# Optimization experiments

Measured on AMD Instinct MI355X. Metric: run time of the kernel, lower is better.

Reference implementation:

```python
import jax, jax.numpy as jnp
import numpy as np

B, V = 256, 2048
PD, MD, H = 1024, 512, 512

def setup_inputs() -> dict:
    key = jax.random.key(0)
    k1, k2, k3, k4, k5 = jax.random.split(key, 5)
    patient_emb = jax.random.normal(k1, (B, PD), dtype=jnp.float32)
    atc4_emb = jax.random.normal(k2, (V, MD), dtype=jnp.float32)
    # Linear(PD+MD -> H): weight (H, PD+MD), bias (H,)
    W1 = jax.random.normal(k3, (H, PD + MD), dtype=jnp.float32) * 0.02
    b1 = jnp.zeros((H,), dtype=jnp.float32)
    # Linear(H -> 1): weight (1, H) -> store as (H,), bias scalar
    w2 = jax.random.normal(k4, (H,), dtype=jnp.float32) * 0.05
    b2 = jnp.zeros((), dtype=jnp.float32)
    return {"patient_emb": patient_emb, "atc4_emb": atc4_emb,
            "W1": W1, "b1": b1, "w2": w2, "b2": b2}

def reference(patient_emb, atc4_emb, W1, b1, w2, b2):
    # Algebraically equivalent to cat([patient, mol]) @ W1.T:
    # split W1 into patient and mol blocks, matmul each, broadcast-add.
    W1p = W1[:, :PD]   # (H, PD)
    W1m = W1[:, PD:]   # (H, MD)
    hp = jnp.einsum('bp,hp->bh', patient_emb, W1p)   # (B, H)
    hm = jnp.einsum('vm,hm->vh', atc4_emb, W1m)      # (V, H)
    h = jnp.tanh(hp[:, None, :] + hm[None, :, :] + b1)  # (B, V, H)
    scores = jnp.einsum('bvh,h->bv', h, w2) + b2     # (B, V)
    return scores
```

## Files before the change

### kernel.cpp

```cpp
#include <hip/hip_runtime.h>
#include <hip/hip_bf16.h>
#include <math.h>

typedef __attribute__((ext_vector_type(8))) short short8;
typedef __attribute__((ext_vector_type(4))) float float4v;
typedef __attribute__((ext_vector_type(2))) float float2v;

__device__ __forceinline__ float2v lo2(float4v v) {
    return __builtin_shufflevector(v, v, 0, 1);
}
__device__ __forceinline__ float2v hi2(float4v v) {
    return __builtin_shufflevector(v, v, 2, 3);
}

__device__ __forceinline__ int2 cvt2bf16x4(float4v v) {
    union { __hip_bfloat162 h2; int i; } u0, u1;
    u0.h2 = __float22bfloat162_rn(make_float2(v.x, v.y));
    u1.h2 = __float22bfloat162_rn(make_float2(v.z, v.w));
    return make_int2(u0.i, u1.i);
}

__global__ __launch_bounds__(256) void gemm_exp(
    const float* __restrict__ patient, const float* __restrict__ atc4,
    const float* __restrict__ W1, const float* __restrict__ b1,
    float* __restrict__ EA, float* __restrict__ EM)
{
    const float* A; const float* W; const float* bias; float* T;
    int lda, K, M;
    if (blockIdx.z == 0) {
        if (blockIdx.x >= 4) return;
        A = patient; lda = 1024; K = 1024; M = 256; bias = b1; T = EA; W = W1;
    } else {
        A = atc4;    lda = 512;  K = 512;  M = 2048; bias = nullptr; T = EM; W = W1 + 1024;
    }
    const int ldw = 1536;

    __shared__ short As[64][72];
    __shared__ short Bs[64][72];
    const int t = threadIdx.x;
    const int m0 = blockIdx.x * 64;
    const int n0 = blockIdx.y * 64;
    const int wave = t >> 6;
    const int lane = t & 63;
    const int wm = (wave & 1) * 32;
    const int wn = (wave >> 1) * 32;
    const int lrow = lane & 15;
    const int quad = lane >> 4;

    float4v acc[2][2];
    #pragma unroll
    for (int i = 0; i < 2; i++)
        #pragma unroll
        for (int j = 0; j < 2; j++)
            acc[i][j] = (float4v){0.f, 0.f, 0.f, 0.f};

    const int sr = t >> 2;
    const int sc = (t & 3) * 16;

    for (int k0 = 0; k0 < K; k0 += 64) {
        const float* ap = A + (size_t)(m0 + sr) * lda + (k0 + sc);
        const float* wp = W + (size_t)(n0 + sr) * ldw + (k0 + sc);
        #pragma unroll
        for (int ii = 0; ii < 4; ii++) {
            float4v av = *(const float4v*)(ap + ii * 4);
            float4v wv = *(const float4v*)(wp + ii * 4);
            *(int2*)&As[sr][sc + ii * 4] = cvt2bf16x4(av);
            *(int2*)&Bs[sr][sc + ii * 4] = cvt2bf16x4(wv);
        }
        __syncthreads();
        #pragma unroll
        for (int kk = 0; kk < 64; kk += 32) {
            short8 af[2], bfr[2];
            #pragma unroll
            for (int i = 0; i < 2; i++)
                af[i] = *(const short8*)&As[wm + i * 16 + lrow][kk + quad * 8];
            #pragma unroll
            for (int j = 0; j < 2; j++)
                bfr[j] = *(const short8*)&Bs[wn + j * 16 + lrow][kk + quad * 8];
            #pragma unroll
            for (int i = 0; i < 2; i++)
                #pragma unroll
                for (int j = 0; j < 2; j++)
                    acc[i][j] = __builtin_amdgcn_mfma_f32_16x16x32_bf16(
                        af[i], bfr[j], acc[i][j], 0, 0, 0);
        }
        __syncthreads();
    }

    #pragma unroll
    for (int i = 0; i < 2; i++) {
        #pragma unroll
        for (int j = 0; j < 2; j++) {
            const int n  = n0 + wn + j * 16 + lrow;
            const int mb = m0 + wm + i * 16 + quad * 4;
            const float bn = bias ? bias[n] : 0.0f;
            float4v ev;
            #pragma unroll
            for (int r = 0; r < 4; r++)
                ev[r] = __expf(2.0f * (acc[i][j][r] + bn));
            *(float4v*)&T[(size_t)n * M + mb] = ev;
        }
    }
}

__device__ __forceinline__ void rat4(
    float2v em0, float2v em1, float2v em2, float2v em3,
    float2v a0, float2v a1, float2v a2, float2v a3,
    float2v c0, float2v c1, float2v c2, float2v c3,
    float2v& acc)
{
    const float2v one2 = {1.f, 1.f};
    float2v d0 = __builtin_elementwise_fma(em0, a0, one2);
    float2v d1 = __builtin_elementwise_fma(em1, a1, one2);
    float2v d2 = __builtin_elementwise_fma(em2, a2, one2);
    float2v d3 = __builtin_elementwise_fma(em3, a3, one2);
    float2v e01 = d0 * d1;
    float2v e23 = d2 * d3;
    float2v n01 = __builtin_elementwise_fma(d1, c0, d0 * c1);
    float2v n23 = __builtin_elementwise_fma(d3, c2, d2 * c3);
    float2v num = __builtin_elementwise_fma(n01, e23, n23 * e01);
    float2v den = e01 * e23;
    float2v r = { __builtin_amdgcn_rcpf(den.x), __builtin_amdgcn_rcpf(den.y) };
    acc = __builtin_elementwise_fma(num, r, acc);
}

__global__ __launch_bounds__(256) void pair_kernel(
    const float* __restrict__ EA, const float* __restrict__ EM,
    const float* __restrict__ w2, float* __restrict__ partial)
{
    __shared__ float sEA[32][68];
    __shared__ float sEM[32][132];
    __shared__ float4v sC4[16];
    const int t  = threadIdx.x;
    const int v0 = blockIdx.x * 128;
    const int b0 = blockIdx.y * 64;
    const int h0 = blockIdx.z * 64;
    const int tx = t & 15;
    const int ty = t >> 4;

    if (t < 16) {
        float4v wv = *(const float4v*)(w2 + h0 + 4 * t);
        sC4[t] = -2.0f * wv;
    }

    float2v accAL[4], accAH[4], accBL[4], accBH[4];
    #pragma unroll
    for (int i = 0; i < 4; i++) {
        accAL[i] = (float2v){0.f, 0.f};  accAH[i] = (float2v){0.f, 0.f};
        accBL[i] = (float2v){0.f, 0.f};  accBH[i] = (float2v){0.f, 0.f};
    }

    const int rS = t >> 3;
    const int cA = (t & 7) * 8;
    const int cM = (t & 7) * 16;

    float4v pA0, pA1, pM0, pM1, pM2, pM3;
    {
        const float* pa = EA + (size_t)(h0 + rS) * 256 + b0 + cA;
        pA0 = *(const float4v*)pa;  pA1 = *(const float4v*)(pa + 4);
        const float* pm = EM + (size_t)(h0 + rS) * 2048 + v0 + cM;
        pM0 = *(const float4v*)pm;       pM1 = *(const float4v*)(pm + 4);
        pM2 = *(const float4v*)(pm + 8); pM3 = *(const float4v*)(pm + 12);
    }
    *(float4v*)&sEA[rS][cA] = pA0;      *(float4v*)&sEA[rS][cA + 4] = pA1;
    *(float4v*)&sEM[rS][cM] = pM0;      *(float4v*)&sEM[rS][cM + 4] = pM1;
    *(float4v*)&sEM[rS][cM + 8] = pM2;  *(float4v*)&sEM[rS][cM + 12] = pM3;
    __syncthreads();
    {
        const float* pa = EA + (size_t)(h0 + 32 + rS) * 256 + b0 + cA;
        pA0 = *(const float4v*)pa;  pA1 = *(const float4v*)(pa + 4);
        const float* pm = EM + (size_t)(h0 + 32 + rS) * 2048 + v0 + cM;
        pM0 = *(const float4v*)pm;       pM1 = *(const float4v*)(pm + 4);
        pM2 = *(const float4v*)(pm + 8); pM3 = *(const float4v*)(pm + 12);
    }

    #pragma unroll
    for (int half = 0; half < 2; half++) {
        #pragma unroll 2
        for (int q = 0; q < 8; q++) {
            const int hq = 4 * q;
            const float4v ea0 = *(const float4v*)&sEA[hq    ][ty * 4];
            const float4v ea1 = *(const float4v*)&sEA[hq + 1][ty * 4];
            const float4v ea2 = *(const float4v*)&sEA[hq + 2][ty * 4];
            const float4v ea3 = *(const float4v*)&sEA[hq + 3][ty * 4];
            const float4v c = sC4[half * 8 + q];
            const float2v c0 = { c.x, c.x };
            const float2v c1 = { c.y, c.y };
            const float2v c2 = { c.z, c.z };
            const float2v c3 = { c.w, c.w };
            {
                const float4v em0 = *(const float4v*)&sEM[hq    ][tx * 4];
                const float4v em1 = *(const float4v*)&sEM[hq + 1][tx * 4];
                const float4v em2 = *(const float4v*)&sEM[hq + 2][tx * 4];
                const float4v em3 = *(const float4v*)&sEM[hq + 3][tx * 4];
                const float2v em0L = lo2(em0), em0H = hi2(em0);
                const float2v em1L = lo2(em1), em1H = hi2(em1);
                const float2v em2L = lo2(em2), em2H = hi2(em2);
                const float2v em3L = lo2(em3), em3H = hi2(em3);
                #pragma unroll
                for (int i = 0; i < 4; i++) {
                    const float2v a0 = { ea0[i], ea0[i] };
                    const float2v a1 = { ea1[i], ea1[i] };
                    const float2v a2 = { ea2[i], ea2[i] };
                    const float2v a3 = { ea3[i], ea3[i] };
                    rat4(em0L, em1L, em2L, em3L, a0, a1, a2, a3,
                         c0, c1, c2, c3, accAL[i]);
                    rat4(em0H, em1H, em2H, em3H, a0, a1, a2, a3,
                         c0, c1, c2, c3, accAH[i]);
                }
            }
            {
                const float4v em0 = *(const float4v*)&sEM[hq    ][64 + tx * 4];
                const float4v em1 = *(const float4v*)&sEM[hq + 1][64 + tx * 4];
                const float4v em2 = *(const float4v*)&sEM[hq + 2][64 + tx * 4];
                const float4v em3 = *(const float4v*)&sEM[hq + 3][64 + tx * 4];
                const float2v em0L = lo2(em0), em0H = hi2(em0);
                const float2v em1L = lo2(em1), em1H = hi2(em1);
                const float2v em2L = lo2(em2), em2H = hi2(em2);
                const float2v em3L = lo2(em3), em3H = hi2(em3);
                #pragma unroll
                for (int i = 0; i < 4; i++) {
                    const float2v a0 = { ea0[i], ea0[i] };
                    const float2v a1 = { ea1[i], ea1[i] };
                    const float2v a2 = { ea2[i], ea2[i] };
                    const float2v a3 = { ea3[i], ea3[i] };
                    rat4(em0L, em1L, em2L, em3L, a0, a1, a2, a3,
                         c0, c1, c2, c3, accBL[i]);
                    rat4(em0H, em1H, em2H, em3H, a0, a1, a2, a3,
                         c0, c1, c2, c3, accBH[i]);
                }
            }
        }
        if (half == 0) {
            __syncthreads();
            *(float4v*)&sEA[rS][cA] = pA0;      *(float4v*)&sEA[rS][cA + 4] = pA1;
            *(float4v*)&sEM[rS][cM] = pM0;      *(float4v*)&sEM[rS][cM + 4] = pM1;
            *(float4v*)&sEM[rS][cM + 8] = pM2;  *(float4v*)&sEM[rS][cM + 12] = pM3;
            __syncthreads();
        }
    }

    float4v w2q = sC4[0];
    #pragma unroll
    for (int k = 1; k < 16; k++) w2q += sC4[k];
    const float w2s = -0.5f * (w2q.x + w2q.y + w2q.z + w2q.w);

    const size_t pb = (size_t)blockIdx.z * (256 * 2048);
    #pragma unroll
    for (int i = 0; i < 4; i++) {
        const size_t row = pb + (size_t)(b0 + ty * 4 + i) * 2048 + v0 + tx * 4;
        float4v oA = { accAL[i].x + w2s, accAL[i].y + w2s,
                       accAH[i].x + w2s, accAH[i].y + w2s };
        float4v oB = { accBL[i].x + w2s, accBL[i].y + w2s,
                       accBH[i].x + w2s, accBH[i].y + w2s };
        *(float4v*)&partial[row] = oA;
        *(float4v*)&partial[row + 64] = oB;
    }
}

__global__ __launch_bounds__(256) void reduce_kernel(
    const float* __restrict__ partial, const float* __restrict__ b2,
    float* __restrict__ out)
{
    const int i = (blockIdx.x * 256 + threadIdx.x) * 4;
    const float bb = b2[0];
    float4v s = *(const float4v*)&partial[i];
    #pragma unroll
    for (int z = 1; z < 8; z++)
        s += *(const float4v*)&partial[(size_t)z * 524288 + i];
    float4v o = s + bb;
    *(float4v*)&out[i] = o;
}

extern "C" void kernel_launch(void* const* d_in, const int* in_sizes, int n_in,
                              void* d_out, int out_size, void* d_ws, size_t ws_size,
                              hipStream_t stream)
{
    const float* patient = (const float*)d_in[0];
    const float* atc4    = (const float*)d_in[1];
    const float* W1      = (const float*)d_in[2];
    const float* b1      = (const float*)d_in[3];
    const float* w2      = (const float*)d_in[4];
    const float* b2      = (const float*)d_in[5];
    float* out = (float*)d_out;
    float* ws  = (float*)d_ws;

    float* EA      = ws;
    float* EM      = ws + 131072;
    float* partial = ws + 1179648;

    gemm_exp<<<dim3(32, 8, 2), 256, 0, stream>>>(patient, atc4, W1, b1, EA, EM);
    pair_kernel<<<dim3(16, 4, 8), 256, 0, stream>>>(EA, EM, w2, partial);
    reduce_kernel<<<512, 256, 0, stream>>>(partial, b2, out);
}
```

Before: 117.9 us.

## Register-prefetch GEMM tiles and halve pair-kernel H split with deeper pipeline

The GEMM kernel now loads the next K-tile of A and W into registers before the MFMA loop, so global latency overlaps with compute. The pair kernel covers 128 hidden units per block instead of 64, in a four-stage rolled loop that prefetches the next slice while computing the current one. This halves the partial buffer written and read by the reduction (4 slices instead of 8). The cost is fewer pair-kernel blocks (256 vs 512), which lowers parallelism across the GPU's compute units, plus more register pressure in the GEMM.

```diff
diff --git a/kernel.cpp b/kernel.cpp
--- a/kernel.cpp
+++ b/kernel.cpp
@@ -57,17 +57,33 @@
     const int sr = t >> 2;
     const int sc = (t & 3) * 16;
 
+    float4v av[4], wv[4];
+    {
+        const float* ap = A + (size_t)(m0 + sr) * lda + sc;
+        const float* wp = W + (size_t)(n0 + sr) * ldw + sc;
+        #pragma unroll
+        for (int ii = 0; ii < 4; ii++) {
+            av[ii] = *(const float4v*)(ap + ii * 4);
+            wv[ii] = *(const float4v*)(wp + ii * 4);
+        }
+    }
+
     for (int k0 = 0; k0 < K; k0 += 64) {
-        const float* ap = A + (size_t)(m0 + sr) * lda + (k0 + sc);
-        const float* wp = W + (size_t)(n0 + sr) * ldw + (k0 + sc);
         #pragma unroll
         for (int ii = 0; ii < 4; ii++) {
-            float4v av = *(const float4v*)(ap + ii * 4);
-            float4v wv = *(const float4v*)(wp + ii * 4);
-            *(int2*)&As[sr][sc + ii * 4] = cvt2bf16x4(av);
-            *(int2*)&Bs[sr][sc + ii * 4] = cvt2bf16x4(wv);
+            *(int2*)&As[sr][sc + ii * 4] = cvt2bf16x4(av[ii]);
+            *(int2*)&Bs[sr][sc + ii * 4] = cvt2bf16x4(wv[ii]);
         }
         __syncthreads();
+        if (k0 + 64 < K) {
+            const float* ap = A + (size_t)(m0 + sr) * lda + (k0 + 64 + sc);
+            const float* wp = W + (size_t)(n0 + sr) * ldw + (k0 + 64 + sc);
+            #pragma unroll
+            for (int ii = 0; ii < 4; ii++) {
+                av[ii] = *(const float4v*)(ap + ii * 4);
+                wv[ii] = *(const float4v*)(wp + ii * 4);
+            }
+        }
         #pragma unroll
         for (int kk = 0; kk < 64; kk += 32) {
             short8 af[2], bfr[2];
@@ -130,17 +146,17 @@
 {
     __shared__ float sEA[32][68];
     __shared__ float sEM[32][132];
-    __shared__ float4v sC4[16];
+    __shared__ float4v sC4[32];
     const int t  = threadIdx.x;
     const int v0 = blockIdx.x * 128;
     const int b0 = blockIdx.y * 64;
-    const int h0 = blockIdx.z * 64;
+    const int h0 = blockIdx.z * 128;
     const int tx = t & 15;
     const int ty = t >> 4;
 
-    if (t < 16) {
-        float4v wv = *(const float4v*)(w2 + h0 + 4 * t);
-        sC4[t] = -2.0f * wv;
+    if (t < 32) {
+        float4v wvq = *(const float4v*)(w2 + h0 + 4 * t);
+        sC4[t] = -2.0f * wvq;
     }
 
     float2v accAL[4], accAH[4], accBL[4], accBH[4];
@@ -166,16 +182,17 @@
     *(float4v*)&sEM[rS][cM] = pM0;      *(float4v*)&sEM[rS][cM + 4] = pM1;
     *(float4v*)&sEM[rS][cM + 8] = pM2;  *(float4v*)&sEM[rS][cM + 12] = pM3;
     __syncthreads();
-    {
-        const float* pa = EA + (size_t)(h0 + 32 + rS) * 256 + b0 + cA;
-        pA0 = *(const float4v*)pa;  pA1 = *(const float4v*)(pa + 4);
-        const float* pm = EM + (size_t)(h0 + 32 + rS) * 2048 + v0 + cM;
-        pM0 = *(const float4v*)pm;       pM1 = *(const float4v*)(pm + 4);
-        pM2 = *(const float4v*)(pm + 8); pM3 = *(const float4v*)(pm + 12);
-    }
-
-    #pragma unroll
-    for (int half = 0; half < 2; half++) {
+
+    #pragma unroll 1
+    for (int s = 0; s < 4; s++) {
+        if (s < 3) {
+            const int hr = h0 + (s + 1) * 32 + rS;
+            const float* pa = EA + (size_t)hr * 256 + b0 + cA;
+            pA0 = *(const float4v*)pa;  pA1 = *(const float4v*)(pa + 4);
+            const float* pm = EM + (size_t)hr * 2048 + v0 + cM;
+            pM0 = *(const float4v*)pm;       pM1 = *(const float4v*)(pm + 4);
+            pM2 = *(const float4v*)(pm + 8); pM3 = *(const float4v*)(pm + 12);
+        }
         #pragma unroll 2
         for (int q = 0; q < 8; q++) {
             const int hq = 4 * q;
@@ -183,7 +200,7 @@
             const float4v ea1 = *(const float4v*)&sEA[hq + 1][ty * 4];
             const float4v ea2 = *(const float4v*)&sEA[hq + 2][ty * 4];
             const float4v ea3 = *(const float4v*)&sEA[hq + 3][ty * 4];
-            const float4v c = sC4[half * 8 + q];
+            const float4v c = sC4[s * 8 + q];
             const float2v c0 = { c.x, c.x };
             const float2v c1 = { c.y, c.y };
             const float2v c2 = { c.z, c.z };
@@ -231,7 +248,7 @@
                 }
             }
         }
-        if (half == 0) {
+        if (s < 3) {
             __syncthreads();
             *(float4v*)&sEA[rS][cA] = pA0;      *(float4v*)&sEA[rS][cA + 4] = pA1;
             *(float4v*)&sEM[rS][cM] = pM0;      *(float4v*)&sEM[rS][cM + 4] = pM1;
@@ -242,7 +259,7 @@
 
     float4v w2q = sC4[0];
     #pragma unroll
-    for (int k = 1; k < 16; k++) w2q += sC4[k];
+    for (int k = 1; k < 32; k++) w2q += sC4[k];
     const float w2s = -0.5f * (w2q.x + w2q.y + w2q.z + w2q.w);
 
     const size_t pb = (size_t)blockIdx.z * (256 * 2048);
@@ -266,7 +283,7 @@
     const float bb = b2[0];
     float4v s = *(const float4v*)&partial[i];
     #pragma unroll
-    for (int z = 1; z < 8; z++)
+    for (int z = 1; z < 4; z++)
         s += *(const float4v*)&partial[(size_t)z * 524288 + i];
     float4v o = s + bb;
     *(float4v*)&out[i] = o;
@@ -290,6 +307,6 @@
     float* partial = ws + 1179648;
 
     gemm_exp<<<dim3(32, 8, 2), 256, 0, stream>>>(patient, atc4, W1, b1, EA, EM);
-    pair_kernel<<<dim3(16, 4, 8), 256, 0, stream>>>(EA, EM, w2, partial);
+    pair_kernel<<<dim3(16, 4, 4), 256, 0, stream>>>(EA, EM, w2, partial);
     reduce_kernel<<<512, 256, 0, stream>>>(partial, b2, out);
 }
```

Result: no change. 117.3 us (-0.5%).
